# Kernel tuning notes

Hardware: AMD Instinct MI355X
Metric: run time of the kernel (lower is better)

The kernel has to match this reference:

```python
import math
import jax, jax.numpy as jnp
import numpy as np

B, S, D, H = 4, 2048, 1024, 16
DK = D // H
TINY = 1e-13  # tiny_value_of_dtype(float32) in the original masked_fill


def setup_inputs() -> dict:
    key = jax.random.key(0)
    ks = jax.random.split(key, 12)
    scale = 1.0 / math.sqrt(D)
    inp = {
        "query": jax.random.normal(ks[0], (B, S, D), jnp.float32),
        "key": jax.random.normal(ks[1], (B, S, D), jnp.float32),
        "value": jax.random.normal(ks[2], (B, S, D), jnp.float32),
        "mask": jax.random.randint(ks[3], (B, S, S), 0, 2, jnp.int32),
        "Wq": jax.random.normal(ks[4], (D, D), jnp.float32) * scale,
        "bq": jnp.zeros((D,), jnp.float32),
        "Wk": jax.random.normal(ks[5], (D, D), jnp.float32) * scale,
        "bk": jnp.zeros((D,), jnp.float32),
        "Wv": jax.random.normal(ks[6], (D, D), jnp.float32) * scale,
        "bv": jnp.zeros((D,), jnp.float32),
        "Wo": jax.random.normal(ks[7], (D, D), jnp.float32) * scale,
        "bo": jnp.zeros((D,), jnp.float32),
    }
    return inp


def _split_heads(x):
    # [B, S, D] -> [B, H, S, DK]
    return x.reshape(B, -1, H, DK).transpose(0, 2, 1, 3)


def reference(query, key, value, mask, Wq, bq, Wk, bk, Wv, bv, Wo, bo):
    q = _split_heads(query @ Wq.T + bq)
    k = _split_heads(key @ Wk.T + bk)
    v = _split_heads(value @ Wv.T + bv)
    # scores: [B, H, Sq, Sk]
    scores = jnp.einsum("bhqd,bhkd->bhqk", q, k) / math.sqrt(DK)
    # non-standard mask fill: replace masked positions with TINY (not -inf)
    m = mask[:, None, :, :] == 0  # [B,1,Sq,Sk] broadcast over heads
    scores = jnp.where(m, jnp.float32(TINY), scores)
    p_attn = jax.nn.softmax(scores, axis=-1)
    # dropout is identity in eval/reference mode
    x = jnp.einsum("bhqk,bhkd->bhqd", p_attn, v)
    x = x.transpose(0, 2, 1, 3).reshape(B, -1, D)
    return x @ Wo.T + bo
```

## Files before the change

### kernel.cpp

```cpp
#include <hip/hip_runtime.h>


typedef __attribute__((ext_vector_type(8))) short bf16x8;
typedef __attribute__((ext_vector_type(4))) float f32x4;
typedef __attribute__((ext_vector_type(16))) float f32x16;
typedef __attribute__((ext_vector_type(4))) unsigned short us4;
typedef unsigned long long u64;
typedef unsigned short u16;
typedef unsigned int u32;

#define DEV static __device__ __forceinline__

DEV u16 f2bf(float f) {
  union { float f; unsigned u; } v; v.f = f;
  return (u16)((v.u + 0x7fffu + ((v.u >> 16) & 1u)) >> 16);
}

DEV u32 cvtpk(float lo, float hi) {
  u32 r;
  asm("v_cvt_pk_bf16_f32 %0, %1, %2" : "=v"(r) : "v"(lo), "v"(hi));
  return r;
}

DEV void plswap(u32& x, u32& y) {
  asm("v_permlane32_swap_b32 %0, %1" : "+v"(x), "+v"(y));
}

DEV float fexp2(float x) {
#if __has_builtin(__builtin_amdgcn_exp2f)
  return __builtin_amdgcn_exp2f(x);
#else
  float r;
  asm volatile("v_exp_f32 %0, %1\n\ts_nop 1" : "=v"(r) : "v"(x));
  return r;
#endif
}

DEV int sbfe1(u32 w, int pos) {
#if __has_builtin(__builtin_amdgcn_sbfe)
  return __builtin_amdgcn_sbfe((int)w, pos, 1);
#else
  return ((int)(w << (31 - pos))) >> 31;
#endif
}

DEV float fmask(float s, int m) {
  union { float f; int i; } u; u.f = s; u.i &= m; return u.f;
}

DEV void gl16(const u16* g, u16* l) {
  __builtin_amdgcn_global_load_lds(
      (const __attribute__((address_space(1))) unsigned int*)g,
      (__attribute__((address_space(3))) unsigned int*)l, 16, 0, 0);
}

DEV int swz(int row, int slot) { return slot ^ (row & 7); }

__global__ void prep_kernel(const float4* __restrict__ q, const float4* __restrict__ k,
                            const float4* __restrict__ v, const float4* __restrict__ wq,
                            const float4* __restrict__ wk, const float4* __restrict__ wv,
                            const float4* __restrict__ wo, const int* __restrict__ mask,
                            us4* __restrict__ xq, us4* __restrict__ xk, us4* __restrict__ xv,
                            us4* __restrict__ owq, us4* __restrict__ owk,
                            us4* __restrict__ owv, us4* __restrict__ owo,
                            u64* __restrict__ bits) {
  const int bid = blockIdx.x;
  if (bid < 28672) {
    const float4* src; us4* dst; int base;
    if (bid < 8192)       { src = q;  dst = xq;  base = 0; }
    else if (bid < 16384) { src = k;  dst = xk;  base = 8192; }
    else if (bid < 24576) { src = v;  dst = xv;  base = 16384; }
    else if (bid < 25600) { src = wq; dst = owq; base = 24576; }
    else if (bid < 26624) { src = wk; dst = owk; base = 25600; }
    else if (bid < 27648) { src = wv; dst = owv; base = 26624; }
    else                  { src = wo; dst = owo; base = 27648; }
    const int i = (bid - base) * 256 + threadIdx.x;
    const float4 t = src[i];
    us4 r = {f2bf(t.x), f2bf(t.y), f2bf(t.z), f2bf(t.w)};
    dst[i] = r;
  } else {
    const int i = (bid - 28672) * 256 + threadIdx.x;
    const u64 bm = __ballot(mask[i] != 0);
    if ((threadIdx.x & 63) == 0) bits[i >> 6] = bm;
  }
}

template <int MODE>
DEV void gemm_body(const u16* __restrict__ P, const u16* __restrict__ Q,
                   const float* __restrict__ bias, void* __restrict__ outp,
                   int pr0, int qr0, u16* lsP, u16* lsQ) {
  constexpr int K = 1024;
  const int tid = threadIdx.x;
  const int w = tid >> 6, lane = tid & 63;
  const int wm = w >> 1, wn = w & 1;
  const int lo = lane & 15, hi = lane >> 4;
  const int srow = lane >> 3, sslot = lane & 7;

  f32x4 acc[4][4];
#pragma unroll
  for (int i = 0; i < 4; ++i)
#pragma unroll
    for (int j = 0; j < 4; ++j) acc[i][j] = (f32x4){0.f, 0.f, 0.f, 0.f};

  for (int kt = 0; kt < K; kt += 64) {
#pragma unroll
    for (int j = 0; j < 4; ++j) {
      const int c = w * 4 + j;
      const int row = c * 8 + srow;
      const int gs = swz(row, sslot);
      gl16(P + (pr0 + row) * K + kt + gs * 8, &lsP[c * 512]);
      gl16(Q + (qr0 + row) * K + kt + gs * 8, &lsQ[c * 512]);
    }
    __syncthreads();
#pragma unroll
    for (int kk = 0; kk < 2; ++kk) {
      bf16x8 af[4], bfr[4];
#pragma unroll
      for (int mf = 0; mf < 4; ++mf) {
        const int r = wm * 64 + mf * 16 + lo;
        af[mf] = *(const bf16x8*)&lsP[r * 64 + swz(r, kk * 4 + hi) * 8];
      }
#pragma unroll
      for (int nf = 0; nf < 4; ++nf) {
        const int r = wn * 64 + nf * 16 + lo;
        bfr[nf] = *(const bf16x8*)&lsQ[r * 64 + swz(r, kk * 4 + hi) * 8];
      }
#pragma unroll
      for (int mf = 0; mf < 4; ++mf)
#pragma unroll
        for (int nf = 0; nf < 4; ++nf)
          acc[mf][nf] = __builtin_amdgcn_mfma_f32_16x16x32_bf16(af[mf], bfr[nf], acc[mf][nf], 0, 0, 0);
    }
    __syncthreads();
  }

#pragma unroll
  for (int mf = 0; mf < 4; ++mf) {
#pragma unroll
    for (int nf = 0; nf < 4; ++nf) {
#pragma unroll
      for (int i = 0; i < 4; ++i) {
        const int gm = pr0 + wm * 64 + mf * 16 + hi * 4 + i;
        const int gn = qr0 + wn * 64 + nf * 16 + lo;
        float val = acc[mf][nf][i];
        if constexpr (MODE == 0 || MODE == 3) {
          val += bias[gn];
          if constexpr (MODE == 3) val *= 0.18033688011112042f;
          const int b = gm >> 11, s = gm & 2047, h = gn >> 6, dk = gn & 63;
          ((u16*)outp)[(((b * 16 + h) * 2048 + s) * 64) + dk] = f2bf(val);
        } else if constexpr (MODE == 1) {
          val += bias[gm];
          const int h = gm >> 6, dk = gm & 63, b = gn >> 11, s = gn & 2047;
          ((u16*)outp)[(((b * 16 + h) * 64 + dk) * 2048) + s] = f2bf(val);
        } else {
          val += bias[gn];
          ((float*)outp)[(size_t)gm * 1024 + gn] = val;
        }
      }
    }
  }
}

__launch_bounds__(256)
__global__ void gemm_qkv(const u16* __restrict__ xq, const u16* __restrict__ xk,
                         const u16* __restrict__ xv, const u16* __restrict__ wq,
                         const u16* __restrict__ wk, const u16* __restrict__ wv,
                         const float* __restrict__ bq, const float* __restrict__ bk,
                         const float* __restrict__ bv, u16* __restrict__ q16,
                         u16* __restrict__ k16, u16* __restrict__ vt16) {
  __shared__ u16 lsP[128 * 64];
  __shared__ u16 lsQ[128 * 64];
  const int z = blockIdx.z;
  if (z == 0)      gemm_body<3>(xq, wq, bq, q16,  blockIdx.y * 128, blockIdx.x * 128, lsP, lsQ);
  else if (z == 1) gemm_body<0>(xk, wk, bk, k16,  blockIdx.y * 128, blockIdx.x * 128, lsP, lsQ);
  else             gemm_body<1>(wv, xv, bv, vt16, blockIdx.x * 128, blockIdx.y * 128, lsP, lsQ);
}

__launch_bounds__(256)
__global__ void gemm_out(const u16* __restrict__ P, const u16* __restrict__ Q,
                         const float* __restrict__ bias, float* __restrict__ outp) {
  __shared__ u16 lsP[128 * 64];
  __shared__ u16 lsQ[128 * 64];
  gemm_body<2>(P, Q, bias, outp, blockIdx.y * 128, blockIdx.x * 128, lsP, lsQ);
}

__launch_bounds__(256, 4)
__global__ void attn_kernel(const u16* __restrict__ q16, const u16* __restrict__ k16,
                            const u16* __restrict__ vt16, const u64* __restrict__ mb,
                            u16* __restrict__ x16) {
  __shared__ u16 lsK[2][64 * 64];
  __shared__ u16 lsV[2][64 * 64];
  const int bh = blockIdx.x;
  const int b = bh >> 4, h = bh & 15;
  const int w = threadIdx.x >> 6, lane = threadIdx.x & 63;
  const int l5 = lane & 31, h1 = lane >> 5, l7 = l5 & 7;
  const int h4 = h1 * 4;
  const int q0 = blockIdx.y * 128 + w * 32;
  const u16* qbase = q16 + (size_t)bh * 2048 * 64;
  const u16* kbase = k16 + (size_t)bh * 2048 * 64;
  const u16* vbase = vt16 + (size_t)bh * 64 * 2048;
  const u64* mrow = mb + ((size_t)b * 2048 + q0 + l5) * 32;

  const int srow = lane >> 3, sslot = lane & 7;
  const int c0 = w * 2;

  const f32x16 z16 = (f32x16)(0.f);

  bf16x8 qf[4];
#pragma unroll
  for (int step = 0; step < 4; ++step)
    qf[step] = *(const bf16x8*)&qbase[(q0 + l5) * 64 + step * 16 + h1 * 8];

  f32x16 acc[2];
  acc[0] = z16; acc[1] = z16;
  float lpart = 0.f;

#pragma unroll
  for (int j = 0; j < 2; ++j) {
    const int c = c0 + j, row = c * 8 + srow;
    const int gs = swz(row, sslot) * 8;
    gl16(kbase + row * 64 + gs, &lsK[0][c * 512]);
    gl16(vbase + row * 2048 + gs, &lsV[0][c * 512]);
  }

  for (int t = 0; t < 32; ++t) {
    const int cur = t & 1;
    __syncthreads();

    if (t < 31) {
      const int kv1 = (t + 1) * 64;
#pragma unroll
      for (int j = 0; j < 2; ++j) {
        const int c = c0 + j, row = c * 8 + srow;
        const int gs = swz(row, sslot) * 8;
        gl16(kbase + (kv1 + row) * 64 + gs, &lsK[cur ^ 1][c * 512]);
        gl16(vbase + row * 2048 + kv1 + gs, &lsV[cur ^ 1][c * 512]);
      }
    }

    const u64 mw = mrow[t];

    f32x16 s[2];
#pragma unroll
    for (int f = 0; f < 2; ++f) {
      f32x16 sv = z16;
#pragma unroll
      for (int step = 0; step < 4; ++step) {
        const int row = f * 32 + l5;
        const bf16x8 kf = *(const bf16x8*)&lsK[cur][row * 64 + ((step * 2 + h1) ^ l7) * 8];
        sv = __builtin_amdgcn_mfma_f32_32x32x16_bf16(kf, qf[step], sv, 0, 0, 0);
      }
      s[f] = sv;
    }

#pragma unroll
    for (int f = 0; f < 2; ++f) {
      const u32 wf = ((f == 0) ? (u32)mw : (u32)(mw >> 32)) >> h4;
      float p[16];
#pragma unroll
      for (int r = 0; r < 16; ++r) {
        const int pos = (r & 3) + 8 * (r >> 2);
        const int m = sbfe1(wf, pos);
        p[r] = fexp2(fmask(s[f][r], m));
        lpart += p[r];
      }
      u32 pk[8];
#pragma unroll
      for (int i = 0; i < 4; ++i) {
        pk[2 * i]     = cvtpk(p[4 * i],     p[4 * i + 1]);
        pk[2 * i + 1] = cvtpk(p[4 * i + 2], p[4 * i + 3]);
      }
      plswap(pk[0], pk[2]); plswap(pk[1], pk[3]);
      plswap(pk[4], pk[6]); plswap(pk[5], pk[7]);

#pragma unroll
      for (int mm = 0; mm < 2; ++mm) {
        const int m = f * 2 + mm;
        union { u32 u[4]; bf16x8 v; } pu;
        pu.u[0] = pk[4 * mm]; pu.u[1] = pk[4 * mm + 1];
        pu.u[2] = pk[4 * mm + 2]; pu.u[3] = pk[4 * mm + 3];
#pragma unroll
        for (int db = 0; db < 2; ++db) {
          const int row = db * 32 + l5;
          const bf16x8 vf = *(const bf16x8*)&lsV[cur][row * 64 + ((m * 2 + h1) ^ l7) * 8];
          acc[db] = __builtin_amdgcn_mfma_f32_32x32x16_bf16(vf, pu.v, acc[db], 0, 0, 0);
        }
      }
    }
  }

  const float tot = lpart + __shfl_xor(lpart, 32, 64);
  const float inv = 1.0f / tot;

  u16* orow = x16 + ((size_t)b * 2048 + q0 + l5) * 1024 + h * 64;
#pragma unroll
  for (int db = 0; db < 2; ++db)
#pragma unroll
    for (int r = 0; r < 16; r += 2) {
      const int d = db * 32 + (r & 3) + 8 * (r >> 2) + h4;
      *(u32*)&orow[d] = cvtpk(acc[db][r] * inv, acc[db][r + 1] * inv);
    }
}

extern "C" void kernel_launch(void* const* d_in, const int* in_sizes, int n_in,
                              void* d_out, int out_size, void* d_ws, size_t ws_size,
                              hipStream_t stream) {
  const float* query = (const float*)d_in[0];
  const float* key   = (const float*)d_in[1];
  const float* value = (const float*)d_in[2];
  const int*   mask  = (const int*)d_in[3];
  const float* Wq = (const float*)d_in[4];
  const float* bq = (const float*)d_in[5];
  const float* Wk = (const float*)d_in[6];
  const float* bk = (const float*)d_in[7];
  const float* Wv = (const float*)d_in[8];
  const float* bv = (const float*)d_in[9];
  const float* Wo = (const float*)d_in[10];
  const float* bo = (const float*)d_in[11];

  char* ws = (char*)d_ws;
  const size_t MB = 1024 * 1024;
  u16* xq   = (u16*)(ws + 0);
  u16* xk   = (u16*)(ws + 16 * MB);
  u16* xv   = (u16*)(ws + 32 * MB);
  u16* wq16 = (u16*)(ws + 48 * MB);
  u16* wk16 = (u16*)(ws + 50 * MB);
  u16* wv16 = (u16*)(ws + 52 * MB);
  u16* wo16 = (u16*)(ws + 54 * MB);
  u16* q16  = (u16*)(ws + 56 * MB);
  u16* k16  = (u16*)(ws + 72 * MB);
  u16* vt16 = (u16*)(ws + 88 * MB);
  u64* mbits = (u64*)(ws + 104 * MB);
  u16* x16  = xq;

  prep_kernel<<<94208, 256, 0, stream>>>(
      (const float4*)query, (const float4*)key, (const float4*)value,
      (const float4*)Wq, (const float4*)Wk, (const float4*)Wv, (const float4*)Wo,
      mask, (us4*)xq, (us4*)xk, (us4*)xv,
      (us4*)wq16, (us4*)wk16, (us4*)wv16, (us4*)wo16, mbits);

  gemm_qkv<<<dim3(8, 64, 3), 256, 0, stream>>>(xq, xk, xv, wq16, wk16, wv16,
                                               bq, bk, bv, q16, k16, vt16);

  attn_kernel<<<dim3(64, 16), 256, 0, stream>>>(q16, k16, vt16, mbits, x16);

  gemm_out<<<dim3(8, 64), 256, 0, stream>>>(x16, wo16, bo, (float*)d_out);
}
```

Baseline: 261.0 us.

## Move mask bit-packing into QKV GEMM launch; add MFMA priority and split row-sum accumulators

```diff
diff --git a/kernel.cpp b/kernel.cpp
--- a/kernel.cpp
+++ b/kernel.cpp
@@ -59,30 +59,23 @@
 __global__ void prep_kernel(const float4* __restrict__ q, const float4* __restrict__ k,
                             const float4* __restrict__ v, const float4* __restrict__ wq,
                             const float4* __restrict__ wk, const float4* __restrict__ wv,
-                            const float4* __restrict__ wo, const int* __restrict__ mask,
+                            const float4* __restrict__ wo,
                             us4* __restrict__ xq, us4* __restrict__ xk, us4* __restrict__ xv,
                             us4* __restrict__ owq, us4* __restrict__ owk,
-                            us4* __restrict__ owv, us4* __restrict__ owo,
-                            u64* __restrict__ bits) {
+                            us4* __restrict__ owv, us4* __restrict__ owo) {
   const int bid = blockIdx.x;
-  if (bid < 28672) {
-    const float4* src; us4* dst; int base;
-    if (bid < 8192)       { src = q;  dst = xq;  base = 0; }
-    else if (bid < 16384) { src = k;  dst = xk;  base = 8192; }
-    else if (bid < 24576) { src = v;  dst = xv;  base = 16384; }
-    else if (bid < 25600) { src = wq; dst = owq; base = 24576; }
-    else if (bid < 26624) { src = wk; dst = owk; base = 25600; }
-    else if (bid < 27648) { src = wv; dst = owv; base = 26624; }
-    else                  { src = wo; dst = owo; base = 27648; }
-    const int i = (bid - base) * 256 + threadIdx.x;
-    const float4 t = src[i];
-    us4 r = {f2bf(t.x), f2bf(t.y), f2bf(t.z), f2bf(t.w)};
-    dst[i] = r;
-  } else {
-    const int i = (bid - 28672) * 256 + threadIdx.x;
-    const u64 bm = __ballot(mask[i] != 0);
-    if ((threadIdx.x & 63) == 0) bits[i >> 6] = bm;
-  }
+  const float4* src; us4* dst; int base;
+  if (bid < 8192)       { src = q;  dst = xq;  base = 0; }
+  else if (bid < 16384) { src = k;  dst = xk;  base = 8192; }
+  else if (bid < 24576) { src = v;  dst = xv;  base = 16384; }
+  else if (bid < 25600) { src = wq; dst = owq; base = 24576; }
+  else if (bid < 26624) { src = wk; dst = owk; base = 25600; }
+  else if (bid < 27648) { src = wv; dst = owv; base = 26624; }
+  else                  { src = wo; dst = owo; base = 27648; }
+  const int i = (bid - base) * 256 + threadIdx.x;
+  const float4 t = src[i];
+  us4 r = {f2bf(t.x), f2bf(t.y), f2bf(t.z), f2bf(t.w)};
+  dst[i] = r;
 }
 
 template <int MODE>
@@ -167,12 +160,24 @@
                          const u16* __restrict__ wk, const u16* __restrict__ wv,
                          const float* __restrict__ bq, const float* __restrict__ bk,
                          const float* __restrict__ bv, u16* __restrict__ q16,
-                         u16* __restrict__ k16, u16* __restrict__ vt16) {
+                         u16* __restrict__ k16, u16* __restrict__ vt16,
+                         const int* __restrict__ mask, u64* __restrict__ bits) {
   __shared__ u16 lsP[128 * 64];
   __shared__ u16 lsQ[128 * 64];
   const int z = blockIdx.z;
-  if (z == 0)      gemm_body<3>(xq, wq, bq, q16,  blockIdx.y * 128, blockIdx.x * 128, lsP, lsQ);
-  else if (z == 1) gemm_body<0>(xk, wk, bk, k16,  blockIdx.y * 128, blockIdx.x * 128, lsP, lsQ);
+  if (z == 0) {
+    const int bid = blockIdx.x + 8 * blockIdx.y;
+    const int tid = threadIdx.x;
+#pragma unroll 4
+    for (int it = 0; it < 128; ++it) {
+      const int i = (it * 512 + bid) * 256 + tid;
+      const u64 bm = __ballot(mask[i] != 0);
+      if ((tid & 63) == 0) bits[i >> 6] = bm;
+    }
+    return;
+  }
+  if (z == 1)      gemm_body<3>(xq, wq, bq, q16,  blockIdx.y * 128, blockIdx.x * 128, lsP, lsQ);
+  else if (z == 2) gemm_body<0>(xk, wk, bk, k16,  blockIdx.y * 128, blockIdx.x * 128, lsP, lsQ);
   else             gemm_body<1>(wv, xv, bv, vt16, blockIdx.x * 128, blockIdx.y * 128, lsP, lsQ);
 }
 
@@ -213,7 +218,7 @@
 
   f32x16 acc[2];
   acc[0] = z16; acc[1] = z16;
-  float lpart = 0.f;
+  float lp0 = 0.f, lp1 = 0.f, lp2 = 0.f, lp3 = 0.f;
 
 #pragma unroll
   for (int j = 0; j < 2; ++j) {
@@ -241,6 +246,7 @@
     const u64 mw = mrow[t];
 
     f32x16 s[2];
+    __builtin_amdgcn_s_setprio(1);
 #pragma unroll
     for (int f = 0; f < 2; ++f) {
       f32x16 sv = z16;
@@ -252,6 +258,7 @@
       }
       s[f] = sv;
     }
+    __builtin_amdgcn_s_setprio(0);
 
 #pragma unroll
     for (int f = 0; f < 2; ++f) {
@@ -262,8 +269,11 @@
         const int pos = (r & 3) + 8 * (r >> 2);
         const int m = sbfe1(wf, pos);
         p[r] = fexp2(fmask(s[f][r], m));
-        lpart += p[r];
-      }
+      }
+      lp0 += (p[0] + p[4]) + (p[8] + p[12]);
+      lp1 += (p[1] + p[5]) + (p[9] + p[13]);
+      lp2 += (p[2] + p[6]) + (p[10] + p[14]);
+      lp3 += (p[3] + p[7]) + (p[11] + p[15]);
       u32 pk[8];
 #pragma unroll
       for (int i = 0; i < 4; ++i) {
@@ -279,16 +289,19 @@
         union { u32 u[4]; bf16x8 v; } pu;
         pu.u[0] = pk[4 * mm]; pu.u[1] = pk[4 * mm + 1];
         pu.u[2] = pk[4 * mm + 2]; pu.u[3] = pk[4 * mm + 3];
+        __builtin_amdgcn_s_setprio(1);
 #pragma unroll
         for (int db = 0; db < 2; ++db) {
           const int row = db * 32 + l5;
           const bf16x8 vf = *(const bf16x8*)&lsV[cur][row * 64 + ((m * 2 + h1) ^ l7) * 8];
           acc[db] = __builtin_amdgcn_mfma_f32_32x32x16_bf16(vf, pu.v, acc[db], 0, 0, 0);
         }
-      }
-    }
-  }
-
+        __builtin_amdgcn_s_setprio(0);
+      }
+    }
+  }
+
+  const float lpart = (lp0 + lp1) + (lp2 + lp3);
   const float tot = lpart + __shfl_xor(lpart, 32, 64);
   const float inv = 1.0f / tot;
 
@@ -333,14 +346,15 @@
   u64* mbits = (u64*)(ws + 104 * MB);
   u16* x16  = xq;
 
-  prep_kernel<<<94208, 256, 0, stream>>>(
+  prep_kernel<<<28672, 256, 0, stream>>>(
       (const float4*)query, (const float4*)key, (const float4*)value,
       (const float4*)Wq, (const float4*)Wk, (const float4*)Wv, (const float4*)Wo,
-      mask, (us4*)xq, (us4*)xk, (us4*)xv,
-      (us4*)wq16, (us4*)wk16, (us4*)wv16, (us4*)wo16, mbits);
-
-  gemm_qkv<<<dim3(8, 64, 3), 256, 0, stream>>>(xq, xk, xv, wq16, wk16, wv16,
-                                               bq, bk, bv, q16, k16, vt16);
+      (us4*)xq, (us4*)xk, (us4*)xv,
+      (us4*)wq16, (us4*)wk16, (us4*)wv16, (us4*)wo16);
+
+  gemm_qkv<<<dim3(8, 64, 4), 256, 0, stream>>>(xq, xk, xv, wq16, wk16, wv16,
+                                               bq, bk, bv, q16, k16, vt16,
+                                               mask, mbits);
 
   attn_kernel<<<dim3(64, 16), 256, 0, stream>>>(q16, k16, vt16, mbits, x16);
 
```

Measured after the change: 283.3 us. 1.09x slower.
